# Performance work log

Measured on AMD Instinct MI355X. Metric: run time of the kernel, lower is better.

## Reference

```python
import jax, jax.numpy as jnp
import numpy as np
from jax import lax

B, C, H, W = 4, 64, 256, 256
T, Q = 16, 0.2
C2 = 2 * C


def conv2d(x, w, b, pad):
    y = lax.conv_general_dilated(x, w, (1, 1), [(pad, pad), (pad, pad)],
                                 dimension_numbers=('NCHW', 'OIHW', 'NCHW'))
    return y + b[None, :, None, None]


def setup_inputs() -> dict:
    key = jax.random.key(0)
    ks = jax.random.split(key, 10)
    x = jax.random.normal(ks[0], (B, C, H, W), dtype=jnp.float32)
    lms = jax.random.normal(ks[1], (B, 4, H, W), dtype=jnp.float32)
    # params (kaiming-ish scale)
    W_conv = jax.random.normal(ks[2], (C2, C, 3, 3), dtype=jnp.float32) * (1.0 / np.sqrt(C * 9))
    b_conv = jnp.zeros((C2,), dtype=jnp.float32)
    W_out = jax.random.normal(ks[3], (4, C2), dtype=jnp.float32) * (1.0 / np.sqrt(C2))  # 1x1 conv as matrix
    b_out = jnp.zeros((4,), dtype=jnp.float32)
    W_aue = jax.random.normal(ks[4], (4, C2, 3, 3), dtype=jnp.float32) * (1.0 / np.sqrt(C2 * 9))
    b_aue = jnp.zeros((4,), dtype=jnp.float32)
    # T Bernoulli(1-q) channel masks, fixed for reproducibility  [T, 2C]
    masks = jax.random.bernoulli(ks[5], 1.0 - Q, (T, C2)).astype(jnp.float32)
    return {"x": x, "lms": lms, "W_conv": W_conv, "b_conv": b_conv,
            "W_out": W_out, "b_out": b_out, "W_aue": W_aue, "b_aue": b_aue,
            "masks": masks}


def reference(x, lms, W_conv, b_conv, W_out, b_out, W_aue, b_aue, masks):
    # feature extraction: 3x3 conv C -> 2C
    h = conv2d(x, W_conv, b_conv, 1)                      # [B, 2C, H, W]
    # MC-dropout samples: out(mask_t * h) == (W_out * mask_t) @ h  (1x1 conv is linear)
    Wt = W_out[None, :, :] * masks[:, None, :]            # [T, 4, 2C]
    samples = jnp.tanh(jnp.einsum('toc,bchw->tbohw', Wt, h)
                       + b_out[None, None, :, None, None]) + lms[None]  # [T, B, 4, H, W]
    mean = jnp.mean(samples, axis=0)
    EU = jnp.var(samples, axis=0, ddof=1)                 # unbiased variance over T
    AU = jax.nn.sigmoid(conv2d(h, W_aue, b_aue, 1))       # [B, 4, H, W]
    return (AU, EU, mean)
```

## Files before the change

### kernel.cpp

```cpp
#include <hip/hip_runtime.h>

#define Bsz 4
#define Cin 64
#define C2c 128
#define Hh 256
#define Ww 256
#define Tt 16
#define HW (Hh*Ww)
#define PLANE (Bsz*4*HW)

typedef __attribute__((ext_vector_type(8))) short bf16x8;
typedef __attribute__((ext_vector_type(4))) float f32x4;

#define H_OFF   0
#define XT_OFF  67108864
#define WBF_OFF 100663296
#define WTB_OFF 100810752
#define AUB_OFF 100827136

__device__ __forceinline__ unsigned short f2bf(float f) {
  union { float f; unsigned u; } cv; cv.f = f;
  unsigned u = cv.u;
  unsigned r = (u + 0x7fffu + ((u >> 16) & 1u)) >> 16;
  return (unsigned short)r;
}

union U8 { uint2 u2[2]; uint4 u4; bf16x8 v; };

__global__ void wtb_kernel(const float* __restrict__ W_out,
                           const float* __restrict__ masks,
                           unsigned short* __restrict__ Wtb) {
  int i = blockIdx.x * 256 + threadIdx.x;
  if (i < 64 * C2c) {
    int to = i >> 7, c = i & 127;
    int t = to >> 2, o = to & 3;
    Wtb[i] = f2bf(W_out[o * C2c + c] * masks[t * C2c + c]);
  }
}

__global__ void wpack_kernel(const float* __restrict__ Wc, unsigned short* __restrict__ Wbf) {
  int idx = blockIdx.x * 256 + threadIdx.x;
  if (idx < 18 * 8 * 64 * 8) {
    int j = idx & 7;
    int lane = (idx >> 3) & 63;
    int nt = (idx >> 9) & 7;
    int c = idx >> 12;
    int q = lane >> 4;
    int tap = c >> 1;
    int ic = (c & 1) * 32 + q * 8 + j;
    int n = nt * 16 + (lane & 15);
    Wbf[idx] = f2bf(Wc[((size_t)n * Cin + ic) * 9 + tap]);
  }
}

__global__ void aupack_kernel(const float* __restrict__ W_aue, unsigned short* __restrict__ Aub) {
  int i = blockIdx.x * 256 + threadIdx.x;
  if (i < 16 * 1152) {
    int m = i / 1152, k = i % 1152;
    int tap = k >> 7, c = k & 127;
    float v = (m < 4) ? W_aue[((size_t)m * C2c + c) * 9 + tap] : 0.f;
    Aub[i] = f2bf(v);
  }
}

__global__ __launch_bounds__(256) void xt_kernel(const float* __restrict__ x,
                                                 unsigned short* __restrict__ xT) {
  __shared__ unsigned short xs[64][65];
  const int tid = threadIdx.x;
  const int x0 = blockIdx.x * 64, y = blockIdx.y, bi = blockIdx.z;
  const int tx = tid & 63, ti = tid >> 6;
  #pragma unroll
  for (int i = 0; i < 16; ++i) {
    int ic = ti * 16 + i;
    float v = x[(((size_t)bi * Cin + ic) * Hh + y) * Ww + x0 + tx];
    xs[ic][tx] = f2bf(v);
  }
  __syncthreads();
  const int icg = tid & 7, xl = tid >> 3;
  #pragma unroll
  for (int rep = 0; rep < 2; ++rep) {
    int xx = xl + 32 * rep;
    unsigned short u[8];
    #pragma unroll
    for (int k = 0; k < 8; ++k) u[k] = xs[icg * 8 + k][xx];
    *(uint4*)(xT + (((size_t)bi * Hh + y) * Ww + (x0 + xx)) * Cin + icg * 8) = *(uint4*)u;
  }
}

__global__ __launch_bounds__(256, 3) void conv1_mfma(
    const unsigned short* __restrict__ xT, const unsigned short* __restrict__ Wbf,
    const float* __restrict__ bc, unsigned short* __restrict__ hout) {
  __shared__ unsigned short At[10 * 18 * 68];
  const int tid = threadIdx.x;
  const int x0 = blockIdx.x * 16, y0 = blockIdx.y * 8, bi = blockIdx.z;

  for (int g = tid; g < 10 * 18 * 8; g += 256) {
    int icg = g & 7;
    int rx = (g >> 3) % 18;
    int ry = g / (18 * 8);
    int gy = y0 - 1 + ry, gx = x0 - 1 + rx;
    uint2 lo = make_uint2(0, 0), hi = make_uint2(0, 0);
    if ((unsigned)gy < Hh && (unsigned)gx < Ww) {
      uint4 v = *(const uint4*)(xT + (((size_t)bi * Hh + gy) * Ww + gx) * Cin + icg * 8);
      lo.x = v.x; lo.y = v.y; hi.x = v.z; hi.y = v.w;
    }
    int e = (ry * 18 + rx) * 68 + icg * 8;
    *(uint2*)(&At[e]) = lo;
    *(uint2*)(&At[e + 4]) = hi;
  }
  __syncthreads();

  const int lane = tid & 63, wv = tid >> 6;
  const int wo = wv & 1, wy = wv >> 1;
  const int n16 = lane & 15, q = lane >> 4;

  f32x4 acc[4][4];
  #pragma unroll
  for (int i = 0; i < 4; ++i)
    #pragma unroll
    for (int j = 0; j < 4; ++j) acc[i][j] = (f32x4){0.f, 0.f, 0.f, 0.f};

  #pragma unroll
  for (int c = 0; c < 18; ++c) {
    const int tap = c >> 1, ichalf = (c & 1) * 32;
    const int dy = tap / 3, dx = tap % 3;
    bf16x8 wfr[4];
    const unsigned short* wb = Wbf + ((size_t)(c * 8 + wo * 4) * 64 + lane) * 8;
    #pragma unroll
    for (int i = 0; i < 4; ++i)
      wfr[i] = ((const U8*)(wb + i * 512))->v;
    bf16x8 xfr[4];
    const int ebase = ((wy * 4 + dy) * 18 + n16 + dx) * 68 + ichalf + q * 8;
    #pragma unroll
    for (int j = 0; j < 4; ++j) {
      U8 t;
      t.u2[0] = *(const uint2*)(&At[ebase + j * (18 * 68)]);
      t.u2[1] = *(const uint2*)(&At[ebase + j * (18 * 68) + 4]);
      xfr[j] = t.v;
    }
    #pragma unroll
    for (int i = 0; i < 4; ++i)
      #pragma unroll
      for (int j = 0; j < 4; ++j)
        acc[i][j] = __builtin_amdgcn_mfma_f32_16x16x32_bf16(wfr[i], xfr[j], acc[i][j], 0, 0, 0);
  }

  #pragma unroll
  for (int i = 0; i < 4; ++i) {
    const int ocb = (wo * 4 + i) * 16 + q * 4;
    const float4 b4 = *(const float4*)(bc + ocb);
    #pragma unroll
    for (int j = 0; j < 4; ++j) {
      const int y = y0 + wy * 4 + j;
      ushort4 o4;
      o4.x = f2bf(acc[i][j][0] + b4.x);
      o4.y = f2bf(acc[i][j][1] + b4.y);
      o4.z = f2bf(acc[i][j][2] + b4.z);
      o4.w = f2bf(acc[i][j][3] + b4.w);
      *(ushort4*)(hout + (((size_t)bi * Hh + y) * Ww + x0 + n16) * C2c + ocb) = o4;
    }
  }
}

#define S2P 132
__global__ __launch_bounds__(256, 3) void stage2_mfma(
    const unsigned short* __restrict__ h, const unsigned short* __restrict__ Wtb,
    const unsigned short* __restrict__ Aub, const float* __restrict__ b_out,
    const float* __restrict__ b_aue, const float* __restrict__ lms,
    float* __restrict__ out) {
  __shared__ unsigned short ht[10 * 18 * S2P];
  const int tid = threadIdx.x;
  const int x0 = blockIdx.x * 16, y0 = blockIdx.y * 8, bi = blockIdx.z;
  const unsigned short* hb = h + (size_t)bi * HW * C2c;

  for (int g = tid; g < 10 * 18 * 16; g += 256) {
    int part = g & 15;
    int rx = (g >> 4) % 18;
    int ry = g / (18 * 16);
    int gy = y0 - 1 + ry, gx = x0 - 1 + rx;
    uint2 lo = make_uint2(0, 0), hi = make_uint2(0, 0);
    if ((unsigned)gy < Hh && (unsigned)gx < Ww) {
      uint4 v = *(const uint4*)(hb + ((size_t)gy * Ww + gx) * C2c + part * 8);
      lo.x = v.x; lo.y = v.y; hi.x = v.z; hi.y = v.w;
    }
    int e = (ry * 18 + rx) * S2P + part * 8;
    *(uint2*)(&ht[e]) = lo;
    *(uint2*)(&ht[e + 4]) = hi;
  }
  __syncthreads();

  const int lane = tid & 63, wv = tid >> 6;
  const int n16 = lane & 15, q = lane >> 4;

  f32x4 accG[2][4];
  f32x4 accA[2];
  #pragma unroll
  for (int nt = 0; nt < 2; ++nt) {
    accA[nt] = (f32x4){0.f, 0.f, 0.f, 0.f};
    #pragma unroll
    for (int mt = 0; mt < 4; ++mt) accG[nt][mt] = (f32x4){0.f, 0.f, 0.f, 0.f};
  }

  #pragma unroll
  for (int kc = 0; kc < 4; ++kc) {
    bf16x8 afr[4];
    #pragma unroll
    for (int mt = 0; mt < 4; ++mt)
      afr[mt] = ((const U8*)(Wtb + (size_t)(mt * 16 + n16) * C2c + kc * 32 + q * 8))->v;
    #pragma unroll
    for (int nt = 0; nt < 2; ++nt) {
      int e = ((wv * 2 + nt + 1) * 18 + n16 + 1) * S2P + kc * 32 + q * 8;
      U8 b;
      b.u2[0] = *(const uint2*)(&ht[e]);
      b.u2[1] = *(const uint2*)(&ht[e + 4]);
      #pragma unroll
      for (int mt = 0; mt < 4; ++mt)
        accG[nt][mt] = __builtin_amdgcn_mfma_f32_16x16x32_bf16(afr[mt], b.v, accG[nt][mt], 0, 0, 0);
    }
  }

  #pragma unroll
  for (int kc = 0; kc < 36; ++kc) {
    const int tap = kc >> 2, co = (kc & 3) * 32;
    const int dy = tap / 3, dx = tap % 3;
    bf16x8 afr = ((const U8*)(Aub + (size_t)n16 * 1152 + kc * 32 + q * 8))->v;
    #pragma unroll
    for (int nt = 0; nt < 2; ++nt) {
      int e = ((wv * 2 + nt + dy) * 18 + n16 + dx) * S2P + co + q * 8;
      U8 b;
      b.u2[0] = *(const uint2*)(&ht[e]);
      b.u2[1] = *(const uint2*)(&ht[e + 4]);
      accA[nt] = __builtin_amdgcn_mfma_f32_16x16x32_bf16(afr, b.v, accA[nt], 0, 0, 0);
    }
  }

  const float b0 = b_out[0], b1 = b_out[1], b2 = b_out[2], b3 = b_out[3];
  const float ba = b_aue[q];
  const int px = x0 + n16;
  #pragma unroll
  for (int nt = 0; nt < 2; ++nt) {
    const int y = y0 + wv * 2 + nt;
    float th[4][4];
    #pragma unroll
    for (int mt = 0; mt < 4; ++mt) {
      #pragma unroll
      for (int r = 0; r < 4; ++r) {
        float bo = (r == 0) ? b0 : (r == 1) ? b1 : (r == 2) ? b2 : b3;
        float v = accG[nt][mt][r] + bo;
        float e = __expf(2.f * v);
        th[mt][r] = 1.f - 2.f / (e + 1.f);
      }
    }
    float mean_r[4], eu_r[4];
    #pragma unroll
    for (int r = 0; r < 4; ++r) {
      float s = th[0][r] + th[1][r] + th[2][r] + th[3][r];
      s += __shfl_xor(s, 16);
      s += __shfl_xor(s, 32);
      float m = s * (1.f / 16.f);
      float d0 = th[0][r] - m, d1 = th[1][r] - m, d2 = th[2][r] - m, d3 = th[3][r] - m;
      float vs = d0 * d0 + d1 * d1 + d2 * d2 + d3 * d3;
      vs += __shfl_xor(vs, 16);
      vs += __shfl_xor(vs, 32);
      mean_r[r] = m;
      eu_r[r] = vs * (1.f / 15.f);
    }
    float au_r[4];
    #pragma unroll
    for (int r = 0; r < 4; ++r) au_r[r] = __shfl(accA[nt][r], n16);

    float m_q  = (q == 0) ? mean_r[0] : (q == 1) ? mean_r[1] : (q == 2) ? mean_r[2] : mean_r[3];
    float eu_q = (q == 0) ? eu_r[0]   : (q == 1) ? eu_r[1]   : (q == 2) ? eu_r[2]   : eu_r[3];
    float au_q = (q == 0) ? au_r[0]   : (q == 1) ? au_r[1]   : (q == 2) ? au_r[2]   : au_r[3];
    au_q = 1.f / (1.f + __expf(-(au_q + ba)));
    size_t oidx = ((size_t)(bi * 4 + q)) * HW + (size_t)y * Ww + px;
    float lm = lms[oidx];
    out[oidx] = au_q;
    out[PLANE + oidx] = eu_q;
    out[2 * (size_t)PLANE + oidx] = m_q + lm;
  }
}

extern "C" void kernel_launch(void* const* d_in, const int* in_sizes, int n_in,
                              void* d_out, int out_size, void* d_ws, size_t ws_size,
                              hipStream_t stream) {
  const float* x      = (const float*)d_in[0];
  const float* lms    = (const float*)d_in[1];
  const float* W_conv = (const float*)d_in[2];
  const float* b_conv = (const float*)d_in[3];
  const float* W_out  = (const float*)d_in[4];
  const float* b_out  = (const float*)d_in[5];
  const float* W_aue  = (const float*)d_in[6];
  const float* b_aue  = (const float*)d_in[7];
  const float* masks  = (const float*)d_in[8];
  float* out = (float*)d_out;

  char* ws = (char*)d_ws;
  unsigned short* h   = (unsigned short*)(ws + H_OFF);
  unsigned short* xT  = (unsigned short*)(ws + XT_OFF);
  unsigned short* Wbf = (unsigned short*)(ws + WBF_OFF);
  unsigned short* Wtb = (unsigned short*)(ws + WTB_OFF);
  unsigned short* Aub = (unsigned short*)(ws + AUB_OFF);

  wtb_kernel<<<dim3(32), dim3(256), 0, stream>>>(W_out, masks, Wtb);
  wpack_kernel<<<dim3(288), dim3(256), 0, stream>>>(W_conv, Wbf);
  aupack_kernel<<<dim3(72), dim3(256), 0, stream>>>(W_aue, Aub);
  xt_kernel<<<dim3(4, 256, 4), dim3(256), 0, stream>>>(x, xT);
  conv1_mfma<<<dim3(16, 32, 4), dim3(256), 0, stream>>>(xT, Wbf, b_conv, h);
  stage2_mfma<<<dim3(16, 32, 4), dim3(256), 0, stream>>>(h, Wtb, Aub, b_out, b_aue, lms, out);
}
```

Before: 265.9 us.

## Fuse conv1 into stage2 with halo recompute; merge weight-prep kernels

The 3x3 feature conv and the stage-2 kernel (dropout-sample GEMM plus AU conv) become one kernel. Each block computes h for its 10x18 halo region directly into LDS, padded to 192 pixels, then runs the stage-2 MFMAs from that LDS tile. This removes the global write and re-read of the full bf16 h tensor. The cost is about 1.5x the conv1 MFMA work for the halo, plus a larger LDS footprint that may limit occupancy. The three small weight-packing kernels are also merged into a single launch.

```diff
diff --git a/kernel.cpp b/kernel.cpp
--- a/kernel.cpp
+++ b/kernel.cpp
@@ -12,11 +12,13 @@
 typedef __attribute__((ext_vector_type(8))) short bf16x8;
 typedef __attribute__((ext_vector_type(4))) float f32x4;
 
-#define H_OFF   0
-#define XT_OFF  67108864
-#define WBF_OFF 100663296
-#define WTB_OFF 100810752
-#define AUB_OFF 100827136
+#define XT_OFF  0
+#define WBF_OFF 33554432
+#define WTB_OFF 33701888
+#define AUB_OFF 33718272
+
+#define XP 76
+#define HP 132
 
 __device__ __forceinline__ unsigned short f2bf(float f) {
   union { float f; unsigned u; } cv; cv.f = f;
@@ -27,20 +29,17 @@
 
 union U8 { uint2 u2[2]; uint4 u4; bf16x8 v; };
 
-__global__ void wtb_kernel(const float* __restrict__ W_out,
-                           const float* __restrict__ masks,
-                           unsigned short* __restrict__ Wtb) {
+__global__ void prep_kernel(const float* __restrict__ W_out, const float* __restrict__ masks,
+                            const float* __restrict__ Wc, const float* __restrict__ W_aue,
+                            unsigned short* __restrict__ Wtb, unsigned short* __restrict__ Wbf,
+                            unsigned short* __restrict__ Aub) {
   int i = blockIdx.x * 256 + threadIdx.x;
-  if (i < 64 * C2c) {
+  if (i < 8192) {
     int to = i >> 7, c = i & 127;
     int t = to >> 2, o = to & 3;
     Wtb[i] = f2bf(W_out[o * C2c + c] * masks[t * C2c + c]);
-  }
-}
-
-__global__ void wpack_kernel(const float* __restrict__ Wc, unsigned short* __restrict__ Wbf) {
-  int idx = blockIdx.x * 256 + threadIdx.x;
-  if (idx < 18 * 8 * 64 * 8) {
+  } else if (i < 8192 + 73728) {
+    int idx = i - 8192;
     int j = idx & 7;
     int lane = (idx >> 3) & 63;
     int nt = (idx >> 9) & 7;
@@ -50,16 +49,12 @@
     int ic = (c & 1) * 32 + q * 8 + j;
     int n = nt * 16 + (lane & 15);
     Wbf[idx] = f2bf(Wc[((size_t)n * Cin + ic) * 9 + tap]);
-  }
-}
-
-__global__ void aupack_kernel(const float* __restrict__ W_aue, unsigned short* __restrict__ Aub) {
-  int i = blockIdx.x * 256 + threadIdx.x;
-  if (i < 16 * 1152) {
-    int m = i / 1152, k = i % 1152;
+  } else if (i < 8192 + 73728 + 18432) {
+    int idx = i - 8192 - 73728;
+    int m = idx / 1152, k = idx % 1152;
     int tap = k >> 7, c = k & 127;
     float v = (m < 4) ? W_aue[((size_t)m * C2c + c) * 9 + tap] : 0.f;
-    Aub[i] = f2bf(v);
+    Aub[idx] = f2bf(v);
   }
 }
 
@@ -87,110 +82,99 @@
   }
 }
 
-__global__ __launch_bounds__(256, 3) void conv1_mfma(
+__global__ __launch_bounds__(256, 3) void fused_kernel(
     const unsigned short* __restrict__ xT, const unsigned short* __restrict__ Wbf,
-    const float* __restrict__ bc, unsigned short* __restrict__ hout) {
-  __shared__ unsigned short At[10 * 18 * 68];
+    const unsigned short* __restrict__ Wtb, const unsigned short* __restrict__ Aub,
+    const float* __restrict__ bc, const float* __restrict__ b_out,
+    const float* __restrict__ b_aue, const float* __restrict__ lms,
+    float* __restrict__ out) {
+  __shared__ unsigned short sh[192 * HP];
   const int tid = threadIdx.x;
   const int x0 = blockIdx.x * 16, y0 = blockIdx.y * 8, bi = blockIdx.z;
 
-  for (int g = tid; g < 10 * 18 * 8; g += 256) {
+  for (int g = tid; g < 12 * 20 * 8; g += 256) {
     int icg = g & 7;
-    int rx = (g >> 3) % 18;
-    int ry = g / (18 * 8);
-    int gy = y0 - 1 + ry, gx = x0 - 1 + rx;
+    int xc = (g >> 3) % 20;
+    int xr = g / 160;
+    int gy = y0 - 2 + xr, gx = x0 - 2 + xc;
     uint2 lo = make_uint2(0, 0), hi = make_uint2(0, 0);
     if ((unsigned)gy < Hh && (unsigned)gx < Ww) {
       uint4 v = *(const uint4*)(xT + (((size_t)bi * Hh + gy) * Ww + gx) * Cin + icg * 8);
       lo.x = v.x; lo.y = v.y; hi.x = v.z; hi.y = v.w;
     }
-    int e = (ry * 18 + rx) * 68 + icg * 8;
-    *(uint2*)(&At[e]) = lo;
-    *(uint2*)(&At[e + 4]) = hi;
+    int e = (xr * 20 + xc) * XP + icg * 8;
+    *(uint2*)(&sh[e]) = lo;
+    *(uint2*)(&sh[e + 4]) = hi;
   }
   __syncthreads();
 
   const int lane = tid & 63, wv = tid >> 6;
-  const int wo = wv & 1, wy = wv >> 1;
   const int n16 = lane & 15, q = lane >> 4;
 
-  f32x4 acc[4][4];
-  #pragma unroll
-  for (int i = 0; i < 4; ++i)
-    #pragma unroll
-    for (int j = 0; j < 4; ++j) acc[i][j] = (f32x4){0.f, 0.f, 0.f, 0.f};
+  int xbase[3];
+  #pragma unroll
+  for (int s = 0; s < 3; ++s) {
+    int px = (wv * 3 + s) * 16 + n16;
+    int pr = px / 18, pc = px % 18;
+    xbase[s] = (pr * 20 + pc) * XP + q * 8;
+  }
+
+  f32x4 acc[3][8];
+  #pragma unroll
+  for (int s = 0; s < 3; ++s)
+    #pragma unroll
+    for (int mt = 0; mt < 8; ++mt) acc[s][mt] = (f32x4){0.f, 0.f, 0.f, 0.f};
 
   #pragma unroll
   for (int c = 0; c < 18; ++c) {
     const int tap = c >> 1, ichalf = (c & 1) * 32;
     const int dy = tap / 3, dx = tap % 3;
-    bf16x8 wfr[4];
-    const unsigned short* wb = Wbf + ((size_t)(c * 8 + wo * 4) * 64 + lane) * 8;
-    #pragma unroll
-    for (int i = 0; i < 4; ++i)
-      wfr[i] = ((const U8*)(wb + i * 512))->v;
-    bf16x8 xfr[4];
-    const int ebase = ((wy * 4 + dy) * 18 + n16 + dx) * 68 + ichalf + q * 8;
-    #pragma unroll
-    for (int j = 0; j < 4; ++j) {
+    const int xoff = (dy * 20 + dx) * XP + ichalf;
+    bf16x8 xfr[3];
+    #pragma unroll
+    for (int s = 0; s < 3; ++s) {
       U8 t;
-      t.u2[0] = *(const uint2*)(&At[ebase + j * (18 * 68)]);
-      t.u2[1] = *(const uint2*)(&At[ebase + j * (18 * 68) + 4]);
-      xfr[j] = t.v;
-    }
-    #pragma unroll
-    for (int i = 0; i < 4; ++i)
-      #pragma unroll
-      for (int j = 0; j < 4; ++j)
-        acc[i][j] = __builtin_amdgcn_mfma_f32_16x16x32_bf16(wfr[i], xfr[j], acc[i][j], 0, 0, 0);
-  }
-
-  #pragma unroll
-  for (int i = 0; i < 4; ++i) {
-    const int ocb = (wo * 4 + i) * 16 + q * 4;
-    const float4 b4 = *(const float4*)(bc + ocb);
-    #pragma unroll
-    for (int j = 0; j < 4; ++j) {
-      const int y = y0 + wy * 4 + j;
+      int e = xbase[s] + xoff;
+      t.u2[0] = *(const uint2*)(&sh[e]);
+      t.u2[1] = *(const uint2*)(&sh[e + 4]);
+      xfr[s] = t.v;
+    }
+    #pragma unroll
+    for (int mh = 0; mh < 2; ++mh) {
+      bf16x8 wfr[4];
+      const unsigned short* wb = Wbf + ((size_t)(c * 8 + mh * 4) * 64 + lane) * 8;
+      #pragma unroll
+      for (int i4 = 0; i4 < 4; ++i4)
+        wfr[i4] = ((const U8*)(wb + i4 * 512))->v;
+      #pragma unroll
+      for (int s = 0; s < 3; ++s)
+        #pragma unroll
+        for (int i4 = 0; i4 < 4; ++i4)
+          acc[s][mh * 4 + i4] =
+            __builtin_amdgcn_mfma_f32_16x16x32_bf16(wfr[i4], xfr[s], acc[s][mh * 4 + i4], 0, 0, 0);
+    }
+  }
+  __syncthreads();
+
+  #pragma unroll
+  for (int s = 0; s < 3; ++s) {
+    const int px = (wv * 3 + s) * 16 + n16;
+    const int pr = px / 18, pc = px % 18;
+    const int gy = y0 - 1 + pr, gx = x0 - 1 + pc;
+    const bool valid = ((unsigned)gy < Hh) && ((unsigned)gx < Ww);
+    #pragma unroll
+    for (int mt = 0; mt < 8; ++mt) {
+      const int oc0 = mt * 16 + q * 4;
+      const float4 b4 = *(const float4*)(bc + oc0);
       ushort4 o4;
-      o4.x = f2bf(acc[i][j][0] + b4.x);
-      o4.y = f2bf(acc[i][j][1] + b4.y);
-      o4.z = f2bf(acc[i][j][2] + b4.z);
-      o4.w = f2bf(acc[i][j][3] + b4.w);
-      *(ushort4*)(hout + (((size_t)bi * Hh + y) * Ww + x0 + n16) * C2c + ocb) = o4;
-    }
-  }
-}
-
-#define S2P 132
-__global__ __launch_bounds__(256, 3) void stage2_mfma(
-    const unsigned short* __restrict__ h, const unsigned short* __restrict__ Wtb,
-    const unsigned short* __restrict__ Aub, const float* __restrict__ b_out,
-    const float* __restrict__ b_aue, const float* __restrict__ lms,
-    float* __restrict__ out) {
-  __shared__ unsigned short ht[10 * 18 * S2P];
-  const int tid = threadIdx.x;
-  const int x0 = blockIdx.x * 16, y0 = blockIdx.y * 8, bi = blockIdx.z;
-  const unsigned short* hb = h + (size_t)bi * HW * C2c;
-
-  for (int g = tid; g < 10 * 18 * 16; g += 256) {
-    int part = g & 15;
-    int rx = (g >> 4) % 18;
-    int ry = g / (18 * 16);
-    int gy = y0 - 1 + ry, gx = x0 - 1 + rx;
-    uint2 lo = make_uint2(0, 0), hi = make_uint2(0, 0);
-    if ((unsigned)gy < Hh && (unsigned)gx < Ww) {
-      uint4 v = *(const uint4*)(hb + ((size_t)gy * Ww + gx) * C2c + part * 8);
-      lo.x = v.x; lo.y = v.y; hi.x = v.z; hi.y = v.w;
-    }
-    int e = (ry * 18 + rx) * S2P + part * 8;
-    *(uint2*)(&ht[e]) = lo;
-    *(uint2*)(&ht[e + 4]) = hi;
-  }
-  __syncthreads();
-
-  const int lane = tid & 63, wv = tid >> 6;
-  const int n16 = lane & 15, q = lane >> 4;
+      o4.x = valid ? f2bf(acc[s][mt][0] + b4.x) : (unsigned short)0;
+      o4.y = valid ? f2bf(acc[s][mt][1] + b4.y) : (unsigned short)0;
+      o4.z = valid ? f2bf(acc[s][mt][2] + b4.z) : (unsigned short)0;
+      o4.w = valid ? f2bf(acc[s][mt][3] + b4.w) : (unsigned short)0;
+      *(ushort4*)(&sh[px * HP + oc0]) = o4;
+    }
+  }
+  __syncthreads();
 
   f32x4 accG[2][4];
   f32x4 accA[2];
@@ -209,10 +193,10 @@
       afr[mt] = ((const U8*)(Wtb + (size_t)(mt * 16 + n16) * C2c + kc * 32 + q * 8))->v;
     #pragma unroll
     for (int nt = 0; nt < 2; ++nt) {
-      int e = ((wv * 2 + nt + 1) * 18 + n16 + 1) * S2P + kc * 32 + q * 8;
+      int e = (((wv * 2 + nt) + 1) * 18 + n16 + 1) * HP + kc * 32 + q * 8;
       U8 b;
-      b.u2[0] = *(const uint2*)(&ht[e]);
-      b.u2[1] = *(const uint2*)(&ht[e + 4]);
+      b.u2[0] = *(const uint2*)(&sh[e]);
+      b.u2[1] = *(const uint2*)(&sh[e + 4]);
       #pragma unroll
       for (int mt = 0; mt < 4; ++mt)
         accG[nt][mt] = __builtin_amdgcn_mfma_f32_16x16x32_bf16(afr[mt], b.v, accG[nt][mt], 0, 0, 0);
@@ -226,10 +210,10 @@
     bf16x8 afr = ((const U8*)(Aub + (size_t)n16 * 1152 + kc * 32 + q * 8))->v;
     #pragma unroll
     for (int nt = 0; nt < 2; ++nt) {
-      int e = ((wv * 2 + nt + dy) * 18 + n16 + dx) * S2P + co + q * 8;
+      int e = ((wv * 2 + nt + dy) * 18 + n16 + dx) * HP + co + q * 8;
       U8 b;
-      b.u2[0] = *(const uint2*)(&ht[e]);
-      b.u2[1] = *(const uint2*)(&ht[e + 4]);
+      b.u2[0] = *(const uint2*)(&sh[e]);
+      b.u2[1] = *(const uint2*)(&sh[e + 4]);
       accA[nt] = __builtin_amdgcn_mfma_f32_16x16x32_bf16(afr, b.v, accA[nt], 0, 0, 0);
     }
   }
@@ -296,16 +280,13 @@
   float* out = (float*)d_out;
 
   char* ws = (char*)d_ws;
-  unsigned short* h   = (unsigned short*)(ws + H_OFF);
   unsigned short* xT  = (unsigned short*)(ws + XT_OFF);
   unsigned short* Wbf = (unsigned short*)(ws + WBF_OFF);
   unsigned short* Wtb = (unsigned short*)(ws + WTB_OFF);
   unsigned short* Aub = (unsigned short*)(ws + AUB_OFF);
 
-  wtb_kernel<<<dim3(32), dim3(256), 0, stream>>>(W_out, masks, Wtb);
-  wpack_kernel<<<dim3(288), dim3(256), 0, stream>>>(W_conv, Wbf);
-  aupack_kernel<<<dim3(72), dim3(256), 0, stream>>>(W_aue, Aub);
+  prep_kernel<<<dim3(392), dim3(256), 0, stream>>>(W_out, masks, W_conv, W_aue, Wtb, Wbf, Aub);
   xt_kernel<<<dim3(4, 256, 4), dim3(256), 0, stream>>>(x, xT);
-  conv1_mfma<<<dim3(16, 32, 4), dim3(256), 0, stream>>>(xT, Wbf, b_conv, h);
-  stage2_mfma<<<dim3(16, 32, 4), dim3(256), 0, stream>>>(h, Wtb, Aub, b_out, b_aue, lms, out);
-}
+  fused_kernel<<<dim3(16, 32, 4), dim3(256), 0, stream>>>(xT, Wbf, Wtb, Aub, b_conv,
+                                                          b_out, b_aue, lms, out);
+}
```

Result: faster. 223.7 us (-15.9%).
